# Kernel optimization log

Hardware: AMD Instinct MI355X
Metric: run time of the kernel (lower is better)

The kernel has to match this reference:

```python
import jax, jax.numpy as jnp
import numpy as np

B, T, IN, H, OUT = 4096, 256, 2, 50, 2


def _rnn_layer(x, W_ih, W_hh, b_ih, b_hh):
    # x: [B, T, F] -> out: [B, T, H]. Elman RNN: h_t = tanh(W_ih x_t + b_ih + W_hh h_{t-1} + b_hh)
    pre = jnp.einsum('btf,hf->bth', x, W_ih) + b_ih + b_hh  # input projection hoisted out of scan
    h0 = jnp.zeros((x.shape[0], W_hh.shape[0]), dtype=x.dtype)

    def step(h, pre_t):
        h = jnp.tanh(pre_t + h @ W_hh.T)
        return h, h

    _, hs = jax.lax.scan(step, h0, jnp.swapaxes(pre, 0, 1))  # scan over time: [T, B, H]
    return jnp.swapaxes(hs, 0, 1)


def setup_inputs() -> dict:
    key = jax.random.key(0)
    ks = jax.random.split(key, 16)
    s_in = 1.0 / np.sqrt(H)  # torch nn.RNN init: U(-1/sqrt(H), 1/sqrt(H))

    def u(k, shape):
        return jax.random.uniform(k, shape, jnp.float32, -s_in, s_in)

    return {
        'x': jax.random.normal(ks[0], (B, T, IN), jnp.float32),
        'W_ih1': u(ks[1], (H, IN)), 'W_hh1': u(ks[2], (H, H)), 'b_ih1': u(ks[3], (H,)), 'b_hh1': u(ks[4], (H,)),
        'W_ih2': u(ks[5], (H, H)), 'W_hh2': u(ks[6], (H, H)), 'b_ih2': u(ks[7], (H,)), 'b_hh2': u(ks[8], (H,)),
        'W_ih3': u(ks[9], (H, H)), 'W_hh3': u(ks[10], (H, H)), 'b_ih3': u(ks[11], (H,)), 'b_hh3': u(ks[12], (H,)),
        'fc_w': u(ks[13], (OUT, H)), 'fc_b': u(ks[14], (OUT,)),
    }


def reference(x, W_ih1, W_hh1, b_ih1, b_hh1, W_ih2, W_hh2, b_ih2, b_hh2,
              W_ih3, W_hh3, b_ih3, b_hh3, fc_w, fc_b):
    out = _rnn_layer(x, W_ih1, W_hh1, b_ih1, b_hh1)
    out = _rnn_layer(out, W_ih2, W_hh2, b_ih2, b_hh2)
    out = _rnn_layer(out, W_ih3, W_hh3, b_ih3, b_hh3)
    return out[:, -1, :] @ fc_w.T + fc_b  # [B, OUT]
```

## Files before the change

kernel.cpp:

```cpp
#include <hip/hip_runtime.h>
#include <hip/hip_fp16.h>

namespace {

constexpr int T_STEPS = 256;
constexpr int HD = 50;
constexpr int HP = 64;
constexpr int KST = 88;
constexpr int KSTS = 72;
constexpr int BT = 16;
constexpr int NTHR = 768;
constexpr int XST = 34;
constexpr int LAY_SH = BT * KST;
constexpr int SLOT_SH = 3 * LAY_SH;

typedef __attribute__((ext_vector_type(8))) _Float16 f16x8;
typedef __attribute__((ext_vector_type(4))) float f32x4;

__device__ __forceinline__ unsigned short f2h(float x) {
  __half h = __float2half(x);
  return *reinterpret_cast<unsigned short*>(&h);
}
__device__ __forceinline__ float h2f(unsigned short u) {
  __half h;
  *reinterpret_cast<unsigned short*>(&h) = u;
  return __half2float(h);
}

#define MFMA16 __builtin_amdgcn_mfma_f32_16x16x32_f16

__device__ __forceinline__ void barrier_nodrain() {
  asm volatile("s_barrier" ::: "memory");
}

__global__ __launch_bounds__(NTHR, 3) void rnn3_kernel(
    const float* __restrict__ x,
    const float* __restrict__ Wih1, const float* __restrict__ Whh1,
    const float* __restrict__ bih1, const float* __restrict__ bhh1,
    const float* __restrict__ Wih2, const float* __restrict__ Whh2,
    const float* __restrict__ bih2, const float* __restrict__ bhh2,
    const float* __restrict__ Wih3, const float* __restrict__ Whh3,
    const float* __restrict__ bih3, const float* __restrict__ bhh3,
    const float* __restrict__ fcw, const float* __restrict__ fcb,
    float* __restrict__ out) {
  __shared__ unsigned short hbuf[3 * SLOT_SH];
  __shared__ float xls[T_STEPS][XST];
  __shared__ unsigned short scr[HP * KSTS];

  const int tid = threadIdx.x;
  const int w = tid >> 6;
  const int myL = w >> 2;
  const int wv = w & 3;
  const int lane = tid & 63;
  const int quad = lane >> 4;
  const int l15 = lane & 15;
  const int b0 = blockIdx.x * BT;

  {
    unsigned int* hz = reinterpret_cast<unsigned int*>(hbuf);
    const int n = 3 * SLOT_SH / 2;
    for (int i = tid; i < n; i += NTHR) hz[i] = 0u;
  }
  for (int idx = tid; idx < BT * T_STEPS; idx += NTHR) {
    int b = idx >> 8, t = idx & 255;
    float2 v = *reinterpret_cast<const float2*>(x + (size_t)(b0 + b) * (T_STEPS * 2) + 2 * t);
    xls[t][2 * b] = v.x;
    xls[t][2 * b + 1] = v.y;
  }

  const float* mats[5] = {Whh1, Wih2, Whh2, Wih3, Whh3};
  constexpr int matL[5] = {0, 1, 1, 2, 2};
  constexpr int matS[5] = {0, 0, 1, 0, 1};
  f16x8 wA[2][2];
#pragma unroll
  for (int sl = 0; sl < 2; ++sl)
#pragma unroll
    for (int ks = 0; ks < 2; ++ks) wA[sl][ks] = f16x8(0);

  const int arow = 16 * wv + l15;
#pragma unroll
  for (int m = 0; m < 5; ++m) {
    __syncthreads();
    const float* W = mats[m];
    for (int idx = tid; idx < HP * HP; idx += NTHR) {
      int i = idx >> 6, k = idx & 63;
      float v = (i < HD && k < HD) ? W[i * HD + k] : 0.0f;
      scr[i * KSTS + k] = f2h(v);
    }
    __syncthreads();
    if (myL == matL[m]) {
      const int sl = matS[m];
      const unsigned short* ph = &scr[arow * KSTS + 8 * quad];
      wA[sl][0] = *reinterpret_cast<const f16x8*>(ph);
      wA[sl][1] = *reinterpret_cast<const f16x8*>(ph + 32);
    }
  }

  const int ic = 16 * wv + 4 * quad;
  const float* bi = (myL == 0) ? bih1 : (myL == 1) ? bih2 : bih3;
  const float* bh = (myL == 0) ? bhh1 : (myL == 1) ? bhh2 : bhh3;
  float wx0[4], wx1[4];
  f32x4 bsv;
#pragma unroll
  for (int r = 0; r < 4; ++r) {
    int i = ic + r;
    bool v = i < HD;
    bsv[r] = v ? (bi[i] + bh[i]) : 0.0f;
    wx0[r] = (v && myL == 0) ? Wih1[i * 2 + 0] : 0.0f;
    wx1[r] = (v && myL == 0) ? Wih1[i * 2 + 1] : 0.0f;
  }

  const int selfBuf = myL;
  const int crossBuf = (myL > 0) ? myL - 1 : 0;
  const int ldsOff = l15 * KST + 8 * quad;

  const unsigned short* sbase = hbuf + selfBuf * LAY_SH + ldsOff;
  const unsigned short* cbase = hbuf + crossBuf * LAY_SH + ldsOff;
  unsigned short* wbase = hbuf + myL * LAY_SH + l15 * KST + ic;

  f16x8 pfC0 = f16x8(0), pfC1 = f16x8(0);

  __syncthreads();

  auto core = [&](int s, int wr, int rd) {
    f16x8 bS0 = *reinterpret_cast<const f16x8*>(sbase + rd * SLOT_SH);
    f16x8 bS1 = *reinterpret_cast<const f16x8*>(sbase + rd * SLOT_SH + 32);
    f16x8 pfN0, pfN1;
    if (myL > 0) {
      pfN0 = *reinterpret_cast<const f16x8*>(cbase + rd * SLOT_SH);
      pfN1 = *reinterpret_cast<const f16x8*>(cbase + rd * SLOT_SH + 32);
    }
    f32x4 c;
    if (myL == 0) {
      float2 xc = *reinterpret_cast<const float2*>(&xls[s][2 * l15]);
      f32x4 ci;
#pragma unroll
      for (int r = 0; r < 4; ++r) ci[r] = fmaf(wx1[r], xc.y, fmaf(wx0[r], xc.x, bsv[r]));
      c = MFMA16(wA[0][0], bS0, ci, 0, 0, 0);
      c = MFMA16(wA[0][1], bS1, c, 0, 0, 0);
    } else {
      c = MFMA16(wA[0][0], pfC0, bsv, 0, 0, 0);
      c = MFMA16(wA[0][1], pfC1, c, 0, 0, 0);
      c = MFMA16(wA[1][0], bS0, c, 0, 0, 0);
      c = MFMA16(wA[1][1], bS1, c, 0, 0, 0);
    }
    float d[4];
#pragma unroll
    for (int r = 0; r < 4; ++r) {
      float xr = __builtin_amdgcn_fmed3f(c[r], -11.0f, 11.0f);
      d[r] = __expf(2.0f * xr) + 1.0f;
    }
    float p01 = d[0] * d[1], p23 = d[2] * d[3];
    float rp = __builtin_amdgcn_rcpf(p01 * p23);
    float q01 = rp * p23, q23 = rp * p01;
    float iv[4] = {q01 * d[1], q01 * d[0], q23 * d[3], q23 * d[2]};
    unsigned short ht[4];
#pragma unroll
    for (int r = 0; r < 4; ++r) ht[r] = f2h(fmaf(-2.0f, iv[r], 1.0f));
    unsigned int h01 = (unsigned int)ht[0] | ((unsigned int)ht[1] << 16);
    unsigned int h23 = (unsigned int)ht[2] | ((unsigned int)ht[3] << 16);
    *reinterpret_cast<uint2*>(wbase + wr * SLOT_SH) = make_uint2(h01, h23);
    if (myL > 0) { pfC0 = pfN0; pfC1 = pfN1; }
  };

  auto actOf = [&](int s) {
    return (myL == 0) ? (s < T_STEPS)
         : (myL == 1) ? (s >= 2 && s < T_STEPS + 2)
                      : (s >= 4);
  };

  auto stepB = [&](int s, int wr, int rd, bool act) {
    if (act) core(s, wr, rd);
    else if (myL > 0) {
      pfC0 = *reinterpret_cast<const f16x8*>(cbase + rd * SLOT_SH);
      pfC1 = *reinterpret_cast<const f16x8*>(cbase + rd * SLOT_SH + 32);
    }
    __syncthreads();
  };

  for (int s = 0; s < 4; ++s) stepB(s, s % 3, (s + 2) % 3, actOf(s));
  for (int sb = 4; sb < 256; sb += 3) {
    core(sb + 0, 1, 0); barrier_nodrain();
    core(sb + 1, 2, 1); barrier_nodrain();
    core(sb + 2, 0, 2); barrier_nodrain();
  }
  __syncthreads();
  for (int s = 256; s < 260; ++s) stepB(s, s % 3, (s + 2) % 3, actOf(s));

  if (tid < BT * 2) {
    int b = tid >> 1, o = tid & 1;
    const unsigned short* h3 = hbuf + 1 * SLOT_SH + 2 * LAY_SH + b * KST;
    float acc = fcb[o];
    for (int i = 0; i < HD; ++i) acc += fcw[o * HD + i] * h2f(h3[i]);
    out[(size_t)(b0 + b) * 2 + o] = acc;
  }
}

}

extern "C" void kernel_launch(void* const* d_in, const int* in_sizes, int n_in,
                              void* d_out, int out_size, void* d_ws, size_t ws_size,
                              hipStream_t stream) {
  const float* x = (const float*)d_in[0];
  const float* Wih1 = (const float*)d_in[1];
  const float* Whh1 = (const float*)d_in[2];
  const float* bih1 = (const float*)d_in[3];
  const float* bhh1 = (const float*)d_in[4];
  const float* Wih2 = (const float*)d_in[5];
  const float* Whh2 = (const float*)d_in[6];
  const float* bih2 = (const float*)d_in[7];
  const float* bhh2 = (const float*)d_in[8];
  const float* Wih3 = (const float*)d_in[9];
  const float* Whh3 = (const float*)d_in[10];
  const float* bih3 = (const float*)d_in[11];
  const float* bhh3 = (const float*)d_in[12];
  const float* fcw = (const float*)d_in[13];
  const float* fcb = (const float*)d_in[14];

  rnn3_kernel<<<4096 / BT, NTHR, 0, stream>>>(x, Wih1, Whh1, bih1, bhh1,
                                              Wih2, Whh2, bih2, bhh2,
                                              Wih3, Whh3, bih3, bhh3,
                                              fcw, fcb, (float*)d_out);
}
```

Measured before the change: 191.1 us.

## Use one wave per layer with four M-tiles and prefetch recurrent state

The block shrinks from 12 waves (4 per layer, 16 hidden rows each) to 3 waves, one per layer, each computing all 64 padded hidden rows as four MFMA M-tiles. Because one wave now writes the whole hidden state, it can read its own new state straight back into registers after writing it, before the barrier. Cross-layer inputs and the next x value are also prefetched at the end of each step. The last tile evaluates tanh for only its 2 valid rows. This cuts barrier participants and the LDS read latency on the serial time chain, at the cost of 4x more work per wave, fewer waves to hide latency, and one SIMD per CU left unused.

```diff
diff --git a/kernel.cpp b/kernel.cpp
--- a/kernel.cpp
+++ b/kernel.cpp
@@ -9,7 +9,7 @@
 constexpr int KST = 88;
 constexpr int KSTS = 72;
 constexpr int BT = 16;
-constexpr int NTHR = 768;
+constexpr int NTHR = 192;
 constexpr int XST = 34;
 constexpr int LAY_SH = BT * KST;
 constexpr int SLOT_SH = 3 * LAY_SH;
@@ -33,7 +33,7 @@
   asm volatile("s_barrier" ::: "memory");
 }
 
-__global__ __launch_bounds__(NTHR, 3) void rnn3_kernel(
+__global__ __launch_bounds__(NTHR, 1) void rnn3_kernel(
     const float* __restrict__ x,
     const float* __restrict__ Wih1, const float* __restrict__ Whh1,
     const float* __restrict__ bih1, const float* __restrict__ bhh1,
@@ -48,18 +48,16 @@
   __shared__ unsigned short scr[HP * KSTS];
 
   const int tid = threadIdx.x;
-  const int w = tid >> 6;
-  const int myL = w >> 2;
-  const int wv = w & 3;
+  const int myL = tid >> 6;
   const int lane = tid & 63;
   const int quad = lane >> 4;
   const int l15 = lane & 15;
   const int b0 = blockIdx.x * BT;
 
   {
-    unsigned int* hz = reinterpret_cast<unsigned int*>(hbuf);
-    const int n = 3 * SLOT_SH / 2;
-    for (int i = tid; i < n; i += NTHR) hz[i] = 0u;
+    uint4* hz = reinterpret_cast<uint4*>(hbuf);
+    const int n = 3 * SLOT_SH * 2 / 16;
+    for (int i = tid; i < n; i += NTHR) hz[i] = make_uint4(0u, 0u, 0u, 0u);
   }
   for (int idx = tid; idx < BT * T_STEPS; idx += NTHR) {
     int b = idx >> 8, t = idx & 255;
@@ -71,96 +69,125 @@
   const float* mats[5] = {Whh1, Wih2, Whh2, Wih3, Whh3};
   constexpr int matL[5] = {0, 1, 1, 2, 2};
   constexpr int matS[5] = {0, 0, 1, 0, 1};
-  f16x8 wA[2][2];
+  f16x8 wA[2][4][2];
 #pragma unroll
   for (int sl = 0; sl < 2; ++sl)
 #pragma unroll
-    for (int ks = 0; ks < 2; ++ks) wA[sl][ks] = f16x8(0);
-
-  const int arow = 16 * wv + l15;
-#pragma unroll
-  for (int m = 0; m < 5; ++m) {
+    for (int m = 0; m < 4; ++m)
+#pragma unroll
+      for (int ks = 0; ks < 2; ++ks) wA[sl][m][ks] = f16x8(0);
+
+#pragma unroll
+  for (int mm = 0; mm < 5; ++mm) {
     __syncthreads();
-    const float* W = mats[m];
+    const float* W = mats[mm];
     for (int idx = tid; idx < HP * HP; idx += NTHR) {
       int i = idx >> 6, k = idx & 63;
       float v = (i < HD && k < HD) ? W[i * HD + k] : 0.0f;
       scr[i * KSTS + k] = f2h(v);
     }
     __syncthreads();
-    if (myL == matL[m]) {
-      const int sl = matS[m];
-      const unsigned short* ph = &scr[arow * KSTS + 8 * quad];
-      wA[sl][0] = *reinterpret_cast<const f16x8*>(ph);
-      wA[sl][1] = *reinterpret_cast<const f16x8*>(ph + 32);
-    }
-  }
-
-  const int ic = 16 * wv + 4 * quad;
+    if (myL == matL[mm]) {
+      const int sl = matS[mm];
+#pragma unroll
+      for (int m = 0; m < 4; ++m) {
+        const unsigned short* ph = &scr[(16 * m + l15) * KSTS + 8 * quad];
+        wA[sl][m][0] = *reinterpret_cast<const f16x8*>(ph);
+        wA[sl][m][1] = *reinterpret_cast<const f16x8*>(ph + 32);
+      }
+    }
+  }
+
   const float* bi = (myL == 0) ? bih1 : (myL == 1) ? bih2 : bih3;
   const float* bh = (myL == 0) ? bhh1 : (myL == 1) ? bhh2 : bhh3;
-  float wx0[4], wx1[4];
-  f32x4 bsv;
-#pragma unroll
-  for (int r = 0; r < 4; ++r) {
-    int i = ic + r;
-    bool v = i < HD;
-    bsv[r] = v ? (bi[i] + bh[i]) : 0.0f;
-    wx0[r] = (v && myL == 0) ? Wih1[i * 2 + 0] : 0.0f;
-    wx1[r] = (v && myL == 0) ? Wih1[i * 2 + 1] : 0.0f;
-  }
-
-  const int selfBuf = myL;
-  const int crossBuf = (myL > 0) ? myL - 1 : 0;
+  f32x4 bsv[4];
+  float wx0[4][4], wx1[4][4];
+#pragma unroll
+  for (int m = 0; m < 4; ++m)
+#pragma unroll
+    for (int r = 0; r < 4; ++r) {
+      int i = 16 * m + 4 * quad + r;
+      bool v = i < HD;
+      bsv[m][r] = v ? (bi[i] + bh[i]) : 0.0f;
+      wx0[m][r] = (v && myL == 0) ? Wih1[i * 2 + 0] : 0.0f;
+      wx1[m][r] = (v && myL == 0) ? Wih1[i * 2 + 1] : 0.0f;
+    }
+
   const int ldsOff = l15 * KST + 8 * quad;
-
-  const unsigned short* sbase = hbuf + selfBuf * LAY_SH + ldsOff;
-  const unsigned short* cbase = hbuf + crossBuf * LAY_SH + ldsOff;
-  unsigned short* wbase = hbuf + myL * LAY_SH + l15 * KST + ic;
-
+  const unsigned short* sbase = hbuf + myL * LAY_SH + ldsOff;
+  const unsigned short* cbase = hbuf + ((myL > 0) ? myL - 1 : 0) * LAY_SH + ldsOff;
+  unsigned short* wb = hbuf + myL * LAY_SH + l15 * KST + 4 * quad;
+
+  f16x8 bS0 = f16x8(0), bS1 = f16x8(0);
   f16x8 pfC0 = f16x8(0), pfC1 = f16x8(0);
+  float2 xpf;
 
   __syncthreads();
+  xpf = *reinterpret_cast<const float2*>(&xls[0][2 * l15]);
+
+  auto prefetch = [&](int s, int wr, int rd) {
+    bS0 = *reinterpret_cast<const f16x8*>(sbase + wr * SLOT_SH);
+    bS1 = *reinterpret_cast<const f16x8*>(sbase + wr * SLOT_SH + 32);
+    if (myL > 0) {
+      pfC0 = *reinterpret_cast<const f16x8*>(cbase + rd * SLOT_SH);
+      pfC1 = *reinterpret_cast<const f16x8*>(cbase + rd * SLOT_SH + 32);
+    } else {
+      xpf = *reinterpret_cast<const float2*>(&xls[(s + 1) & 255][2 * l15]);
+    }
+  };
 
   auto core = [&](int s, int wr, int rd) {
-    f16x8 bS0 = *reinterpret_cast<const f16x8*>(sbase + rd * SLOT_SH);
-    f16x8 bS1 = *reinterpret_cast<const f16x8*>(sbase + rd * SLOT_SH + 32);
-    f16x8 pfN0, pfN1;
-    if (myL > 0) {
-      pfN0 = *reinterpret_cast<const f16x8*>(cbase + rd * SLOT_SH);
-      pfN1 = *reinterpret_cast<const f16x8*>(cbase + rd * SLOT_SH + 32);
-    }
-    f32x4 c;
+    f32x4 cm[4];
     if (myL == 0) {
-      float2 xc = *reinterpret_cast<const float2*>(&xls[s][2 * l15]);
-      f32x4 ci;
-#pragma unroll
-      for (int r = 0; r < 4; ++r) ci[r] = fmaf(wx1[r], xc.y, fmaf(wx0[r], xc.x, bsv[r]));
-      c = MFMA16(wA[0][0], bS0, ci, 0, 0, 0);
-      c = MFMA16(wA[0][1], bS1, c, 0, 0, 0);
+#pragma unroll
+      for (int m = 0; m < 4; ++m) {
+        f32x4 ci;
+#pragma unroll
+        for (int r = 0; r < 4; ++r)
+          ci[r] = fmaf(wx1[m][r], xpf.y, fmaf(wx0[m][r], xpf.x, bsv[m][r]));
+        f32x4 c = MFMA16(wA[0][m][0], bS0, ci, 0, 0, 0);
+        cm[m] = MFMA16(wA[0][m][1], bS1, c, 0, 0, 0);
+      }
     } else {
-      c = MFMA16(wA[0][0], pfC0, bsv, 0, 0, 0);
-      c = MFMA16(wA[0][1], pfC1, c, 0, 0, 0);
-      c = MFMA16(wA[1][0], bS0, c, 0, 0, 0);
-      c = MFMA16(wA[1][1], bS1, c, 0, 0, 0);
-    }
-    float d[4];
-#pragma unroll
-    for (int r = 0; r < 4; ++r) {
-      float xr = __builtin_amdgcn_fmed3f(c[r], -11.0f, 11.0f);
-      d[r] = __expf(2.0f * xr) + 1.0f;
-    }
-    float p01 = d[0] * d[1], p23 = d[2] * d[3];
-    float rp = __builtin_amdgcn_rcpf(p01 * p23);
-    float q01 = rp * p23, q23 = rp * p01;
-    float iv[4] = {q01 * d[1], q01 * d[0], q23 * d[3], q23 * d[2]};
-    unsigned short ht[4];
-#pragma unroll
-    for (int r = 0; r < 4; ++r) ht[r] = f2h(fmaf(-2.0f, iv[r], 1.0f));
-    unsigned int h01 = (unsigned int)ht[0] | ((unsigned int)ht[1] << 16);
-    unsigned int h23 = (unsigned int)ht[2] | ((unsigned int)ht[3] << 16);
-    *reinterpret_cast<uint2*>(wbase + wr * SLOT_SH) = make_uint2(h01, h23);
-    if (myL > 0) { pfC0 = pfN0; pfC1 = pfN1; }
+#pragma unroll
+      for (int m = 0; m < 4; ++m) {
+        f32x4 c = MFMA16(wA[0][m][0], pfC0, bsv[m], 0, 0, 0);
+        c = MFMA16(wA[0][m][1], pfC1, c, 0, 0, 0);
+        c = MFMA16(wA[1][m][0], bS0, c, 0, 0, 0);
+        cm[m] = MFMA16(wA[1][m][1], bS1, c, 0, 0, 0);
+      }
+    }
+#pragma unroll
+    for (int m = 0; m < 3; ++m) {
+      float d[4];
+#pragma unroll
+      for (int r = 0; r < 4; ++r) {
+        float xr = __builtin_amdgcn_fmed3f(cm[m][r], -11.0f, 11.0f);
+        d[r] = __expf(2.0f * xr) + 1.0f;
+      }
+      float p01 = d[0] * d[1], p23 = d[2] * d[3];
+      float rp = __builtin_amdgcn_rcpf(p01 * p23);
+      float q01 = rp * p23, q23 = rp * p01;
+      unsigned short t0 = f2h(fmaf(-2.0f, q01 * d[1], 1.0f));
+      unsigned short t1 = f2h(fmaf(-2.0f, q01 * d[0], 1.0f));
+      unsigned short t2 = f2h(fmaf(-2.0f, q23 * d[3], 1.0f));
+      unsigned short t3 = f2h(fmaf(-2.0f, q23 * d[2], 1.0f));
+      *reinterpret_cast<uint2*>(wb + wr * SLOT_SH + 16 * m) =
+          make_uint2((unsigned)t0 | ((unsigned)t1 << 16),
+                     (unsigned)t2 | ((unsigned)t3 << 16));
+    }
+    {
+      float x0 = __builtin_amdgcn_fmed3f(cm[3][0], -11.0f, 11.0f);
+      float x1 = __builtin_amdgcn_fmed3f(cm[3][1], -11.0f, 11.0f);
+      float d0 = __expf(2.0f * x0) + 1.0f;
+      float d1 = __expf(2.0f * x1) + 1.0f;
+      float rp = __builtin_amdgcn_rcpf(d0 * d1);
+      unsigned short t0 = f2h(fmaf(-2.0f, rp * d1, 1.0f));
+      unsigned short t1 = f2h(fmaf(-2.0f, rp * d0, 1.0f));
+      *reinterpret_cast<uint2*>(wb + wr * SLOT_SH + 48) =
+          make_uint2((unsigned)t0 | ((unsigned)t1 << 16), 0u);
+    }
+    prefetch(s, wr, rd);
   };
 
   auto actOf = [&](int s) {
@@ -171,10 +198,7 @@
 
   auto stepB = [&](int s, int wr, int rd, bool act) {
     if (act) core(s, wr, rd);
-    else if (myL > 0) {
-      pfC0 = *reinterpret_cast<const f16x8*>(cbase + rd * SLOT_SH);
-      pfC1 = *reinterpret_cast<const f16x8*>(cbase + rd * SLOT_SH + 32);
-    }
+    else prefetch(s, wr, rd);
     __syncthreads();
   };
 
```

New measurement: 253.1 us. 32.4% more time.
